# Kernel tuning notes

Measured on AMD Instinct MI355X. Metric: run time of the kernel, lower is better.

The kernel has to match this reference:

```python
import jax, jax.numpy as jnp
import numpy as np

N_FREQS = 64
BLOCK = 8

def setup_inputs() -> dict:
    key = jax.random.key(0)
    k1, _ = jax.random.split(key)
    x = jax.random.normal(k1, (32, 1, 512, 512), dtype=jnp.float32)
    freq_weights = jnp.ones((N_FREQS,), dtype=jnp.float32)
    return {"x": x, "freq_weights": freq_weights}

def reference(x, freq_weights):
    B, C, H, W = x.shape
    ph = (-H) % BLOCK
    pw = (-W) % BLOCK
    x = jnp.pad(x, ((0, 0), (0, 0), (0, ph), (0, pw)))
    H2, W2 = H + ph, W + pw
    Hb, Wb = H2 // BLOCK, W2 // BLOCK
    # [B, C, Hb, Wb, 8, 8] blocks
    xb = x.reshape(B, C, Hb, BLOCK, Wb, BLOCK).transpose(0, 1, 2, 4, 3, 5)
    # batched tiny rfft2 over the last two (8x8) dims -> [..., 8, 5] complex
    xd = jnp.abs(jnp.fft.rfft2(xb.astype(jnp.float32), norm='ortho'))
    xd = xd.reshape(B, C, Hb, Wb, -1)  # 40 freq bins
    n = min(N_FREQS, xd.shape[-1])
    xd = xd[..., :n]
    if n < N_FREQS:
        xd = jnp.pad(xd, ((0, 0),) * 4 + ((0, N_FREQS - n),))
    w = jax.nn.sigmoid(freq_weights)  # [64]
    xd = (xd * w).mean(axis=1)        # channel mean -> [B, Hb, Wb, 64]
    return xd.transpose(0, 3, 1, 2)   # [B, 64, Hb, Wb]
```

## Files before the change

kernel.cpp:

```cpp
#include <hip/hip_runtime.h>
#include <math.h>


#define NBLOCKS (32 * 64 * 64)

__global__ __launch_bounds__(256) void dct_kernel(
    const float* __restrict__ x,
    const float* __restrict__ fw,
    float* __restrict__ out)
{
    __shared__ float wsig[40];
    const int tid = threadIdx.x;
    if (tid < 40) {
        float f = fw[tid];
        wsig[tid] = 1.0f / (1.0f + __expf(-f));
    }
    __syncthreads();

    const int gid = blockIdx.x * 256 + tid;
    const int wb = gid & 63;
    const int hb = (gid >> 6) & 63;
    const int b  = gid >> 12;

    const float* xp = x + ((size_t)b * 512 + (size_t)hb * 8) * 512 + (size_t)wb * 8;

    const float R = 0.70710678118654752440f;
    const float ct[8] = {1.0f,  R, 0.0f, -R, -1.0f, -R,  0.0f,  R};
    const float st[8] = {0.0f,  R, 1.0f,  R,  0.0f, -R, -1.0f, -R};

    float dr[8][5], di[8][5];
    #pragma unroll
    for (int u = 0; u < 8; ++u)
        #pragma unroll
        for (int v = 0; v < 5; ++v) { dr[u][v] = 0.0f; di[u][v] = 0.0f; }

    #pragma unroll
    for (int i = 0; i < 8; ++i) {
        const float4 a  = *reinterpret_cast<const float4*>(xp + (size_t)i * 512);
        const float4 c4 = *reinterpret_cast<const float4*>(xp + (size_t)i * 512 + 4);
        const float row[8] = {a.x, a.y, a.z, a.w, c4.x, c4.y, c4.z, c4.w};

        float cr[5], ci[5];
        #pragma unroll
        for (int v = 0; v < 5; ++v) {
            float sr = 0.0f, si = 0.0f;
            #pragma unroll
            for (int j = 0; j < 8; ++j) {
                const int t = (v * j) & 7;
                sr += row[j] * ct[t];
                si -= row[j] * st[t];
            }
            cr[v] = sr; ci[v] = si;
        }

        #pragma unroll
        for (int u = 0; u < 8; ++u) {
            const int t = (u * i) & 7;
            const float wr = ct[t];
            const float wi = -st[t];
            #pragma unroll
            for (int v = 0; v < 5; ++v) {
                dr[u][v] += cr[v] * wr - ci[v] * wi;
                di[u][v] += cr[v] * wi + ci[v] * wr;
            }
        }
    }

    float* op = out + (((size_t)b * 64) * 64 + (size_t)hb) * 64 + wb;
    #pragma unroll
    for (int u = 0; u < 8; ++u) {
        #pragma unroll
        for (int v = 0; v < 5; ++v) {
            const int k = u * 5 + v;
            const float mag =
                sqrtf(dr[u][v] * dr[u][v] + di[u][v] * di[u][v]) * 0.125f * wsig[k];
            op[(size_t)k * 4096] = mag;
        }
    }
    #pragma unroll
    for (int k = 40; k < 64; ++k) {
        op[(size_t)k * 4096] = 0.0f;
    }
}

extern "C" void kernel_launch(void* const* d_in, const int* in_sizes, int n_in,
                              void* d_out, int out_size, void* d_ws, size_t ws_size,
                              hipStream_t stream)
{
    const float* x  = (const float*)d_in[0];
    const float* fw = (const float*)d_in[1];
    float* out = (float*)d_out;

    dct_kernel<<<dim3(NBLOCKS / 256), dim3(256), 0, stream>>>(x, fw, out);
}
```

Measured before the change: 84.91 us.

## Split 8x8 block FFT across four threads with shared-memory row spectra

Each 8x8 block is now handled by four threads instead of one. Each thread computes butterfly-style row rFFTs for two rows and writes them to a padded shared-memory buffer; after a barrier, each thread computes two output frequency rows (u and u+4) from the column pass, with the twiddle constants specialised per thread. The aim is to cut per-thread register pressure and arithmetic and to raise parallelism and occupancy. In exchange it adds shared-memory traffic, a block barrier and divergent branches on the thread's row index, although that index is uniform within a wavefront.

```diff
diff --git a/kernel.cpp b/kernel.cpp
--- a/kernel.cpp
+++ b/kernel.cpp
@@ -2,83 +2,140 @@
 #include <math.h>
 
 
-#define NBLOCKS (32 * 64 * 64)
+#define R8 0.70710678118654752440f
 
-__global__ __launch_bounds__(256) void dct_kernel(
+__global__ __launch_bounds__(256, 4) void dct_kernel(
     const float* __restrict__ x,
     const float* __restrict__ fw,
     float* __restrict__ out)
 {
+    __shared__ float spec[64 * 65];
     __shared__ float wsig[40];
+
     const int tid = threadIdx.x;
+    const int g   = blockIdx.x;
+    const int b   = g >> 6;
+    const int hb  = g & 63;
+
     if (tid < 40) {
         float f = fw[tid];
         wsig[tid] = 1.0f / (1.0f + __expf(-f));
     }
+
+    const int wb = tid & 63;
+    const int rr = tid >> 6;
+
+    #pragma unroll
+    for (int s = 0; s < 2; ++s) {
+        const int r = rr + 4 * s;
+        const float* xp = x + (((size_t)b * 512) + (size_t)hb * 8 + r) * 512 + (size_t)wb * 8;
+        const float4 A = *reinterpret_cast<const float4*>(xp);
+        const float4 Bv = *reinterpret_cast<const float4*>(xp + 4);
+        const float r0 = A.x, r1 = A.y, r2 = A.z, r3 = A.w;
+        const float r4 = Bv.x, r5 = Bv.y, r6 = Bv.z, r7 = Bv.w;
+
+        const float a04p = r0 + r4, a04m = r0 - r4;
+        const float a26p = r2 + r6, a26m = r2 - r6;
+        const float a15p = r1 + r5, a15m = r1 - r5;
+        const float a37p = r3 + r7, a37m = r3 - r7;
+
+        const float s1 = a04p + a26p, s2 = a15p + a37p;
+        const float t1 = R8 * (a15m - a37m);
+        const float t2 = R8 * (a15m + a37m);
+
+        const float cr0 = s1 + s2;
+        const float cr4 = s1 - s2;
+        const float cr2 = a04p - a26p;
+        const float ci2 = a37p - a15p;
+        const float cr1 = a04m + t1;
+        const float cr3 = a04m - t1;
+        const float ci1 = -(a26m + t2);
+        const float ci3 = a26m - t2;
+
+        float* sp = &spec[wb * 65 + r * 8];
+        sp[0] = cr0;
+        sp[1] = cr1; sp[2] = ci1;
+        sp[3] = cr2; sp[4] = ci2;
+        sp[5] = cr3; sp[6] = ci3;
+        sp[7] = cr4;
+    }
+
     __syncthreads();
 
-    const int gid = blockIdx.x * 256 + tid;
-    const int wb = gid & 63;
-    const int hb = (gid >> 6) & 63;
-    const int b  = gid >> 12;
+    const float* sp = &spec[wb * 65];
 
-    const float* xp = x + ((size_t)b * 512 + (size_t)hb * 8) * 512 + (size_t)wb * 8;
+    float dAr[5], dAi[5], dBr[5], dBi[5];
+    #pragma unroll
+    for (int v = 0; v < 5; ++v) { dAr[v] = dAi[v] = dBr[v] = dBi[v] = 0.0f; }
 
-    const float R = 0.70710678118654752440f;
-    const float ct[8] = {1.0f,  R, 0.0f, -R, -1.0f, -R,  0.0f,  R};
-    const float st[8] = {0.0f,  R, 1.0f,  R,  0.0f, -R, -1.0f, -R};
+#define COL_I(i, CW, SW) do {                                                  \
+    const float c0r = sp[(i)*8+0];                                             \
+    const float c1r = sp[(i)*8+1], c1i = sp[(i)*8+2];                          \
+    const float c2r = sp[(i)*8+3], c2i = sp[(i)*8+4];                          \
+    const float c3r = sp[(i)*8+5], c3i = sp[(i)*8+6];                          \
+    const float c4r = sp[(i)*8+7];                                             \
+    const float cw = (CW), sw = (SW);                                          \
+    const float t0r = c0r*cw;              const float t0i = c0r*sw;           \
+    const float t1r = c1r*cw - c1i*sw;     const float t1i = c1r*sw + c1i*cw;  \
+    const float t2r = c2r*cw - c2i*sw;     const float t2i = c2r*sw + c2i*cw;  \
+    const float t3r = c3r*cw - c3i*sw;     const float t3i = c3r*sw + c3i*cw;  \
+    const float t4r = c4r*cw;              const float t4i = c4r*sw;           \
+    dAr[0] += t0r; dAi[0] += t0i; dAr[1] += t1r; dAi[1] += t1i;                \
+    dAr[2] += t2r; dAi[2] += t2i; dAr[3] += t3r; dAi[3] += t3i;                \
+    dAr[4] += t4r; dAi[4] += t4i;                                              \
+    if ((i) & 1) {                                                             \
+        dBr[0] -= t0r; dBi[0] -= t0i; dBr[1] -= t1r; dBi[1] -= t1i;            \
+        dBr[2] -= t2r; dBi[2] -= t2i; dBr[3] -= t3r; dBi[3] -= t3i;            \
+        dBr[4] -= t4r; dBi[4] -= t4i;                                          \
+    } else {                                                                   \
+        dBr[0] += t0r; dBi[0] += t0i; dBr[1] += t1r; dBi[1] += t1i;            \
+        dBr[2] += t2r; dBi[2] += t2i; dBr[3] += t3r; dBi[3] += t3i;            \
+        dBr[4] += t4r; dBi[4] += t4i;                                          \
+    }                                                                          \
+} while (0)
 
-    float dr[8][5], di[8][5];
+    if (rr == 0) {
+        COL_I(0, 1.0f, 0.0f); COL_I(1, 1.0f, 0.0f);
+        COL_I(2, 1.0f, 0.0f); COL_I(3, 1.0f, 0.0f);
+        COL_I(4, 1.0f, 0.0f); COL_I(5, 1.0f, 0.0f);
+        COL_I(6, 1.0f, 0.0f); COL_I(7, 1.0f, 0.0f);
+    } else if (rr == 1) {
+        COL_I(0, 1.0f, 0.0f);  COL_I(1,  R8, -R8);
+        COL_I(2, 0.0f, -1.0f); COL_I(3, -R8, -R8);
+        COL_I(4, -1.0f, 0.0f); COL_I(5, -R8,  R8);
+        COL_I(6, 0.0f, 1.0f);  COL_I(7,  R8,  R8);
+    } else if (rr == 2) {
+        COL_I(0, 1.0f, 0.0f);  COL_I(1, 0.0f, -1.0f);
+        COL_I(2, -1.0f, 0.0f); COL_I(3, 0.0f, 1.0f);
+        COL_I(4, 1.0f, 0.0f);  COL_I(5, 0.0f, -1.0f);
+        COL_I(6, -1.0f, 0.0f); COL_I(7, 0.0f, 1.0f);
+    } else {
+        COL_I(0, 1.0f, 0.0f);  COL_I(1, -R8, -R8);
+        COL_I(2, 0.0f, 1.0f);  COL_I(3,  R8, -R8);
+        COL_I(4, -1.0f, 0.0f); COL_I(5,  R8,  R8);
+        COL_I(6, 0.0f, -1.0f); COL_I(7, -R8,  R8);
+    }
+#undef COL_I
+
+    float* op = out + ((size_t)b * 64) * 4096 + (size_t)hb * 64 + wb;
+
+    const int uA = rr;
+    const int uB = rr + 4;
     #pragma unroll
-    for (int u = 0; u < 8; ++u)
-        #pragma unroll
-        for (int v = 0; v < 5; ++v) { dr[u][v] = 0.0f; di[u][v] = 0.0f; }
-
-    #pragma unroll
-    for (int i = 0; i < 8; ++i) {
-        const float4 a  = *reinterpret_cast<const float4*>(xp + (size_t)i * 512);
-        const float4 c4 = *reinterpret_cast<const float4*>(xp + (size_t)i * 512 + 4);
-        const float row[8] = {a.x, a.y, a.z, a.w, c4.x, c4.y, c4.z, c4.w};
-
-        float cr[5], ci[5];
-        #pragma unroll
-        for (int v = 0; v < 5; ++v) {
-            float sr = 0.0f, si = 0.0f;
-            #pragma unroll
-            for (int j = 0; j < 8; ++j) {
-                const int t = (v * j) & 7;
-                sr += row[j] * ct[t];
-                si -= row[j] * st[t];
-            }
-            cr[v] = sr; ci[v] = si;
-        }
-
-        #pragma unroll
-        for (int u = 0; u < 8; ++u) {
-            const int t = (u * i) & 7;
-            const float wr = ct[t];
-            const float wi = -st[t];
-            #pragma unroll
-            for (int v = 0; v < 5; ++v) {
-                dr[u][v] += cr[v] * wr - ci[v] * wi;
-                di[u][v] += cr[v] * wi + ci[v] * wr;
-            }
-        }
-    }
-
-    float* op = out + (((size_t)b * 64) * 64 + (size_t)hb) * 64 + wb;
-    #pragma unroll
-    for (int u = 0; u < 8; ++u) {
-        #pragma unroll
-        for (int v = 0; v < 5; ++v) {
-            const int k = u * 5 + v;
-            const float mag =
-                sqrtf(dr[u][v] * dr[u][v] + di[u][v] * di[u][v]) * 0.125f * wsig[k];
-            op[(size_t)k * 4096] = mag;
-        }
+    for (int v = 0; v < 5; ++v) {
+        const int kA = uA * 5 + v;
+        const float magA = sqrtf(dAr[v] * dAr[v] + dAi[v] * dAi[v]) * 0.125f * wsig[kA];
+        op[(size_t)kA * 4096] = magA;
     }
     #pragma unroll
-    for (int k = 40; k < 64; ++k) {
+    for (int v = 0; v < 5; ++v) {
+        const int kB = uB * 5 + v;
+        const float magB = sqrtf(dBr[v] * dBr[v] + dBi[v] * dBi[v]) * 0.125f * wsig[kB];
+        op[(size_t)kB * 4096] = magB;
+    }
+    #pragma unroll
+    for (int m = 0; m < 6; ++m) {
+        const int k = 40 + rr * 6 + m;
         op[(size_t)k * 4096] = 0.0f;
     }
 }
@@ -91,5 +148,5 @@
     const float* fw = (const float*)d_in[1];
     float* out = (float*)d_out;
 
-    dct_kernel<<<dim3(NBLOCKS / 256), dim3(256), 0, stream>>>(x, fw, out);
+    dct_kernel<<<dim3(32 * 64), dim3(256), 0, stream>>>(x, fw, out);
 }
```

New measurement: 84.01 us. Within noise of the previous version (-1.1%).
